# Performance work log

Hardware: AMD Instinct MI355X
Metric: run time of the kernel (lower is better)

The kernel has to match this reference:

```python
import jax, jax.numpy as jnp
import numpy as np

WINDOW = 20
EPS = 1e-08


def setup_inputs() -> dict:
    key = jax.random.key(0)
    k1, _ = jax.random.split(key)
    B, F, T = 16, 257, 8000
    mag = jax.random.uniform(k1, (B, F, T), dtype=jnp.float32)  # magnitudes are nonnegative
    bias = jnp.zeros((1,), dtype=jnp.float32)
    return {"mag": mag, "bias": bias}


def reference(mag, bias):
    # mag: [B, F, T]; causal sliding-window mean over (F, last WINDOW frames).
    B, F, T = mag.shape
    frame_sum = mag.sum(axis=1)  # [B, T] sum over frequency
    # exclusive-prefix-padded cumsum along time -> O(T) windowed sums
    cs = jnp.concatenate([jnp.zeros((B, 1), mag.dtype), jnp.cumsum(frame_sum, axis=1)], axis=1)  # [B, T+1]
    t = jnp.arange(T)
    start = jnp.maximum(0, t - WINDOW + 1)                 # causal clamp at sequence start
    count = ((t - start + 1) * F).astype(mag.dtype)        # valid elements per window
    win_sum = cs[:, t + 1] - cs[:, start]                  # [B, T]
    mean = win_sum / count + bias                          # learnable bias, broadcast [1]
    mean = mean[:, None, :]                                # [B, 1, T]
    norm = mag / (mean + EPS)                              # [B, F, T]
    return norm, mean
```

## Files before the change

kernel.cpp:

```cpp
#include <hip/hip_runtime.h>

#define WINDOW 20
#define EPS 1e-8f

constexpr int B = 16;
constexpr int F = 257;
constexpr int T = 8000;
constexpr int TQ = T / 4;
constexpr int CHUNK_Q = 32;
constexpr int NTILES = (TQ + CHUNK_Q - 1) / CHUNK_Q;

typedef float f32x4 __attribute__((ext_vector_type(4)));

__device__ __forceinline__ void bar_lds() {
  asm volatile("s_waitcnt lgkmcnt(0)" ::: "memory");
  __builtin_amdgcn_s_barrier();
}

__device__ __forceinline__ void nt_store4(float4* p, float4 v) {
  f32x4 w = {v.x, v.y, v.z, v.w};
  __builtin_nontemporal_store(w, (f32x4*)p);
}

__global__ void __launch_bounds__(512) fused_kernel(
    const float* __restrict__ mag, const float* __restrict__ bias,
    float* __restrict__ out_norm, float* __restrict__ out_mean) {

  const int b    = blockIdx.y;
  const int q0   = blockIdx.x * CHUNK_Q;
  const int tid  = threadIdx.x;
  const int q    = tid & (CHUNK_Q - 1);
  const int rg   = tid >> 5;
  const int wave = tid >> 6;
  const int lane = tid & 63;

  const float4* magq = (const float4*)(mag + (size_t)b * F * T);
  float4* outq = (float4*)(out_norm + (size_t)b * F * T);
  const float bs = bias[0];

  __shared__ float4 red[16][CHUNK_Q];
  __shared__ float  cs[20 + CHUNK_Q * 4];
  __shared__ float4 inv4[CHUNK_Q];

  const int qc  = min(CHUNK_Q, TQ - q0);
  const bool act = (q < qc);

  float4 v[16];
  float4 v16 = make_float4(0.f, 0.f, 0.f, 0.f);
  float4 acc = make_float4(0.f, 0.f, 0.f, 0.f);
  if (act) {
    const float4* p = magq + q0 + q;
    #pragma unroll
    for (int it = 0; it < 16; ++it) {
      float4 tv = p[(size_t)((it << 4) + rg) * TQ];
      v[it] = tv;
      acc.x += tv.x; acc.y += tv.y; acc.z += tv.z; acc.w += tv.w;
    }
    if (rg == 0) {
      v16 = p[(size_t)256 * TQ];
      acc.x += v16.x; acc.y += v16.y; acc.z += v16.z; acc.w += v16.w;
    }
  }

  if (wave < 5) {
    int qh = q0 - 5 + wave;
    float4 hs = make_float4(0.f, 0.f, 0.f, 0.f);
    if (qh >= 0) {
      #pragma unroll
      for (int r = 0; r < 4; ++r) {
        float4 tv = magq[(size_t)(lane + (r << 6)) * TQ + qh];
        hs.x += tv.x; hs.y += tv.y; hs.z += tv.z; hs.w += tv.w;
      }
      if (lane == 0) {
        float4 tv = magq[(size_t)256 * TQ + qh];
        hs.x += tv.x; hs.y += tv.y; hs.z += tv.z; hs.w += tv.w;
      }
    }
    #pragma unroll
    for (int off = 32; off > 0; off >>= 1) {
      hs.x += __shfl_down(hs.x, off);
      hs.y += __shfl_down(hs.y, off);
      hs.z += __shfl_down(hs.z, off);
      hs.w += __shfl_down(hs.w, off);
    }
    if (lane == 0) {
      cs[4 * wave + 0] = hs.x;
      cs[4 * wave + 1] = hs.y;
      cs[4 * wave + 2] = hs.z;
      cs[4 * wave + 3] = hs.w;
    }
  }

  red[rg][q] = acc;
  bar_lds();

  if (wave == 0) {
    if (lane < CHUNK_Q) {
      float4 s = make_float4(0.f, 0.f, 0.f, 0.f);
      #pragma unroll
      for (int r = 0; r < 16; ++r) {
        float4 a = red[r][lane];
        s.x += a.x; s.y += a.y; s.z += a.z; s.w += a.w;
      }
      ((float4*)(cs + 20))[lane] = s;
    }
    asm volatile("s_waitcnt lgkmcnt(0)" ::: "memory");
    const int ncols = qc * 4;
    int c = lane * 2;
    if (c < ncols) {
      int t = q0 * 4 + c;
      float ws = 0.f;
      #pragma unroll
      for (int k = 0; k < WINDOW; ++k) ws += cs[20 + c - k];
      int nwin = (t < WINDOW - 1) ? (t + 1) : WINDOW;
      float mean = ws / (float)(nwin * F) + bs;
      out_mean[b * T + t] = mean;
      ((float*)inv4)[c] = 1.0f / (mean + EPS);

      int c1 = c + 1;
      float ws1 = ws + cs[20 + c1] - cs[c1];
      int t1 = t + 1;
      int nwin1 = (t1 < WINDOW - 1) ? (t1 + 1) : WINDOW;
      float mean1 = ws1 / (float)(nwin1 * F) + bs;
      out_mean[b * T + t1] = mean1;
      ((float*)inv4)[c1] = 1.0f / (mean1 + EPS);
    }
  }
  bar_lds();

  if (act) {
    float4 w = inv4[q];
    float4* o = outq + q0 + q;
    #pragma unroll
    for (int it = 0; it < 16; ++it) {
      float4 tv = v[it];
      tv.x *= w.x; tv.y *= w.y; tv.z *= w.z; tv.w *= w.w;
      nt_store4(&o[(size_t)((it << 4) + rg) * TQ], tv);
    }
    if (rg == 0) {
      float4 tv = v16;
      tv.x *= w.x; tv.y *= w.y; tv.z *= w.z; tv.w *= w.w;
      nt_store4(&o[(size_t)256 * TQ], tv);
    }
  }
}

extern "C" void kernel_launch(void* const* d_in, const int* in_sizes, int n_in,
                              void* d_out, int out_size, void* d_ws, size_t ws_size,
                              hipStream_t stream) {
  const float* mag  = (const float*)d_in[0];
  const float* bias = (const float*)d_in[1];
  float* out_norm = (float*)d_out;
  float* out_mean = (float*)d_out + (size_t)B * F * T;

  dim3 grid(NTILES, B);
  fused_kernel<<<grid, 512, 0, stream>>>(mag, bias, out_norm, out_mean);
}
```

Baseline: 49.41 us.

## Remap blocks per XCD for halo L2 locality and hoist halo loads early

Switches to a 1D grid and remaps block IDs so that consecutive time tiles of the same batch land on the same XCD. Neighbouring tiles re-read each other's columns as the causal-window halo, so keeping them together lets those reads hit the shared L2. The halo loads are also issued before the main loads so their latency overlaps. The mapping assumes the number of blocks divides evenly by 8. NTILES=63 and B=16 give 1008 blocks, which divides by 8, so it holds here.

```diff
diff --git a/kernel.cpp b/kernel.cpp
--- a/kernel.cpp
+++ b/kernel.cpp
@@ -9,6 +9,9 @@
 constexpr int TQ = T / 4;
 constexpr int CHUNK_Q = 32;
 constexpr int NTILES = (TQ + CHUNK_Q - 1) / CHUNK_Q;
+constexpr int NBLK = NTILES * B;
+constexpr int NXCD = 8;
+constexpr int PER_XCD = NBLK / NXCD;
 
 typedef float f32x4 __attribute__((ext_vector_type(4)));
 
@@ -26,8 +29,14 @@
     const float* __restrict__ mag, const float* __restrict__ bias,
     float* __restrict__ out_norm, float* __restrict__ out_mean) {
 
-  const int b    = blockIdx.y;
-  const int q0   = blockIdx.x * CHUNK_Q;
+  const int id   = blockIdx.x;
+  const int xcd  = id & (NXCD - 1);
+  const int slot = id >> 3;
+  const int gidx = xcd * PER_XCD + slot;
+  const int bx   = gidx % NTILES;
+  const int b    = gidx / NTILES;
+
+  const int q0   = bx * CHUNK_Q;
   const int tid  = threadIdx.x;
   const int q    = tid & (CHUNK_Q - 1);
   const int rg   = tid >> 5;
@@ -44,6 +53,18 @@
 
   const int qc  = min(CHUNK_Q, TQ - q0);
   const bool act = (q < qc);
+
+  float4 h0, h1, h2, h3, h4;
+  int qh = q0 - 5 + wave;
+  const bool do_halo = (wave < 5) && (qh >= 0);
+  if (do_halo) {
+    const float4* ph = magq + qh;
+    h0 = ph[(size_t)(lane +   0) * TQ];
+    h1 = ph[(size_t)(lane +  64) * TQ];
+    h2 = ph[(size_t)(lane + 128) * TQ];
+    h3 = ph[(size_t)(lane + 192) * TQ];
+    h4 = (lane == 0) ? ph[(size_t)256 * TQ] : make_float4(0.f, 0.f, 0.f, 0.f);
+  }
 
   float4 v[16];
   float4 v16 = make_float4(0.f, 0.f, 0.f, 0.f);
@@ -63,18 +84,12 @@
   }
 
   if (wave < 5) {
-    int qh = q0 - 5 + wave;
     float4 hs = make_float4(0.f, 0.f, 0.f, 0.f);
-    if (qh >= 0) {
-      #pragma unroll
-      for (int r = 0; r < 4; ++r) {
-        float4 tv = magq[(size_t)(lane + (r << 6)) * TQ + qh];
-        hs.x += tv.x; hs.y += tv.y; hs.z += tv.z; hs.w += tv.w;
-      }
-      if (lane == 0) {
-        float4 tv = magq[(size_t)256 * TQ + qh];
-        hs.x += tv.x; hs.y += tv.y; hs.z += tv.z; hs.w += tv.w;
-      }
+    if (do_halo) {
+      hs.x = ((h0.x + h1.x) + (h2.x + h3.x)) + h4.x;
+      hs.y = ((h0.y + h1.y) + (h2.y + h3.y)) + h4.y;
+      hs.z = ((h0.z + h1.z) + (h2.z + h3.z)) + h4.z;
+      hs.w = ((h0.w + h1.w) + (h2.w + h3.w)) + h4.w;
     }
     #pragma unroll
     for (int off = 32; off > 0; off >>= 1) {
@@ -153,6 +168,5 @@
   float* out_norm = (float*)d_out;
   float* out_mean = (float*)d_out + (size_t)B * F * T;
 
-  dim3 grid(NTILES, B);
-  fused_kernel<<<grid, 512, 0, stream>>>(mag, bias, out_norm, out_mean);
+  fused_kernel<<<NBLK, 512, 0, stream>>>(mag, bias, out_norm, out_mean);
 }
```

Result: faster. 45.54 us (-7.8%).
